# Kernel tuning notes

Measured on AMD Instinct MI355X. Metric: run time of the kernel, lower is better.

## Reference

```python
import jax, jax.numpy as jnp
import numpy as np

EPS = 1e-7
TRUNC = 0.5          # truncation level of the robust L1 objective
K_CAND = 64          # max number of piecewise-linear extrema evaluated per row


def _pad_inf(v):
    # (B, n) -> (B, n+2) with -inf / +inf sentinels (torch _pad_inf)
    b = v.shape[0]
    return jnp.concatenate(
        [jnp.full((b, 1), -jnp.inf, v.dtype), v, jnp.full((b, 1), jnp.inf, v.dtype)], axis=-1)


def _pad_cumsum(c):
    # (B, n) -> (B, n+2): leading zero, trailing repeat of last (torch _pad_cumsum)
    return jnp.concatenate([jnp.zeros_like(c[:, :1]), c, c[:, -1:]], axis=-1)


_search_l = jax.vmap(lambda a, v: jnp.searchsorted(a, v, side='left'))
_search_r = jax.vmap(lambda a, v: jnp.searchsorted(a, v, side='right'))


def _align_trunc(x, y, w):
    # Solves min_a sum_i min(TRUNC, w_i * |a*x_i - y_i|) per row. x,y,w: (B, n).
    sign = jnp.sign(x)
    x = x * sign
    y = y * sign
    wx = w * x
    wy = w * y
    ydx = y / jnp.maximum(x, EPS)                       # breakpoints of |a x - y|
    cand_b = (wy - TRUNC) / jnp.maximum(wx, EPS)        # breakpoints where residual hits trunc
    cand_c = (wy + TRUNC) / jnp.maximum(wx, EPS)

    def sorted_cum(v):
        order = jnp.argsort(v, axis=-1)
        vs = jnp.take_along_axis(v, order, axis=-1)
        q = jnp.cumsum(jnp.take_along_axis(wx, order, axis=-1), axis=-1)
        return _pad_inf(vs), _pad_cumsum(q)

    As, QA = sorted_cum(ydx)
    Bs, QB = sorted_cum(cand_b)
    Cs, QC = sorted_cum(cand_c)

    def deriv(search):
        jA = search(As, ydx) - 1
        jB = search(Bs, ydx) - 1
        jC = search(Cs, ydx) - 1
        return (2 * jnp.take_along_axis(QA, jA, axis=-1)
                - jnp.take_along_axis(QB, jB, axis=-1)
                - jnp.take_along_axis(QC, jC, axis=-1))

    left_d = deriv(_search_l)
    right_d = deriv(_search_r)
    is_ext = (left_d < 0) & (right_d >= 0)
    is_ext = is_ext.at[:, 0].set(is_ext[:, 0] | ~jnp.any(is_ext, axis=-1))

    # first K_CAND extrema indices per row (stable sort: extrema=False-key first)
    cand_idx = jnp.argsort(~is_ext, axis=-1, stable=True)[:, :K_CAND]   # (B, K)
    valid = jnp.take_along_axis(is_ext, cand_idx, axis=-1)
    cand_a = jnp.take_along_axis(ydx, cand_idx, axis=-1)                # (B, K)

    # truncated-L1 residual at each candidate a: (B, K)
    res = jnp.sum(
        jnp.minimum(jnp.abs(cand_a[:, :, None] * x[:, None, :] - y[:, None, :]) * w[:, None, :], TRUNC),
        axis=-1)
    res = jnp.where(valid, res, jnp.inf)

    kbest = jnp.argmin(res, axis=-1)                                    # scatter_min equivalent
    loss = jnp.take_along_axis(res, kbest[:, None], axis=-1)[:, 0]
    index = jnp.take_along_axis(cand_idx, kbest[:, None], axis=-1)[:, 0]
    a = (jnp.take_along_axis(y, index[:, None], axis=-1)[:, 0]
         / jnp.maximum(jnp.take_along_axis(x, index[:, None], axis=-1)[:, 0], EPS))
    return a, loss, index


def setup_inputs() -> dict:
    key = jax.random.key(0)
    k1, k2, k3 = jax.random.split(key, 3)
    B, N = 256, 2048
    points_src = jax.random.normal(k1, (B, N, 3), dtype=jnp.float32)
    points_tgt = jax.random.normal(k2, (B, N, 3), dtype=jnp.float32)
    weight = jax.random.uniform(k3, (B, N), dtype=jnp.float32)  # weights >= 0
    return {"points_src": points_src, "points_tgt": points_tgt, "weight": weight}


def reference(points_src, points_tgt, weight):
    # align_points_scale: flatten (..., N, 3) -> (..., 3N), weight broadcast over xyz
    B = points_src.shape[0]
    x = points_src.reshape(B, -1)
    y = points_tgt.reshape(B, -1)
    w = jnp.broadcast_to(weight[..., None], points_src.shape).reshape(B, -1)
    a, loss, index = _align_trunc(x, y, w)
    return a
```

## Files before the change

kernel.cpp:

```cpp
#include <hip/hip_runtime.h>
#include <math.h>

#define NELEM   6144
#define NWEIGHT 2048
#define SORTN   8192
#define NT      1024
#define NWAVE   (NT / 64)
#define KCAND   64
#define DN      6146
#define PERT    (NELEM / NT)
#define CHUNK   (NELEM / NWAVE)
#define QSCALE  32768.0f

#define WINW     5.2e-3f
#define DELTARES 1.5e-3
#define WCAP     384

__device__ __forceinline__ int lb6144(const float* __restrict__ key, float v) {
    int pos = 0;
#pragma unroll
    for (int step = 4096; step > 0; step >>= 1) {
        int np = pos + step;
        if (np <= NELEM && key[np - 1] < v) pos = np;
    }
    return pos;
}

#define CEK(a, b, up) { float lo = fminf(K[a], K[b]), hi = fmaxf(K[a], K[b]); \
                        K[a] = (up) ? lo : hi; K[b] = (up) ? hi : lo; }

__global__ __launch_bounds__(NT, 8)
void pointloss_align_kernel(const float* __restrict__ X,
                            const float* __restrict__ Y,
                            const float* __restrict__ W,
                            float* __restrict__ out)
{
    __shared__ __align__(16) unsigned char s_mem[73744];
    float* s_sort = (float*)s_mem;
    float* s_key  = (float*)s_mem;
    int*   s_dlt  = (int*)  (s_mem + 24576);
    int*   s_dle  = (int*)  (s_mem + 49160);
    float* s_wzf  = (float*)(s_mem + 24576);
    float* s_wy2  = (float*)(s_mem + 49160);

    __shared__ int   s_wtot[2 * NWAVE];
    __shared__ int   s_woff[2 * NWAVE];
    __shared__ int   s_isum[NWAVE];
    __shared__ int   s_cand[KCAND];
    __shared__ float s_res[KCAND];
    __shared__ int   s_wind[WCAP];
    __shared__ float s_wres[WCAP];
    __shared__ int   s_count;
    __shared__ int   s_fb;
    __shared__ float s_wa;
    __shared__ int   s_wcnt;

    const int tid = threadIdx.x;
    const int row = blockIdx.x;
    const float* xb = X + (size_t)row * NELEM;
    const float* yb = Y + (size_t)row * NELEM;
    const float* wb = W + (size_t)row * NWEIGHT;

    float K[8];
    if (tid < NELEM / 8) {
        const int e0 = tid * 8;
        float4 x0 = *(const float4*)(xb + e0);
        float4 x1 = *(const float4*)(xb + e0 + 4);
        float4 y0 = *(const float4*)(yb + e0);
        float4 y1 = *(const float4*)(yb + e0 + 4);
        float xx[8] = {x0.x, x0.y, x0.z, x0.w, x1.x, x1.y, x1.z, x1.w};
        float yy[8] = {y0.x, y0.y, y0.z, y0.w, y1.x, y1.y, y1.z, y1.w};
#pragma unroll
        for (int r = 0; r < 8; ++r) {
            float x = xx[r], y = yy[r];
            float s = (x > 0.f) ? 1.f : ((x < 0.f) ? -1.f : 0.f);
            K[r] = (y * s) / fmaxf(x * s, 1e-7f);
        }
    } else {
#pragma unroll
        for (int r = 0; r < 8; ++r) K[r] = INFINITY;
    }
    if (tid == 0) s_fb = 0;

    CEK(0, 1, true); CEK(2, 3, false); CEK(4, 5, true); CEK(6, 7, false);
    CEK(0, 2, true); CEK(1, 3, true);  CEK(4, 6, false); CEK(5, 7, false);
    CEK(0, 1, true); CEK(2, 3, true);  CEK(4, 5, false); CEK(6, 7, false);
    for (int kk = 8; kk <= 512; kk <<= 1) {
        const bool up = ((tid & (kk >> 3)) == 0);
        for (int jj = kk >> 1; jj >= 8; jj >>= 1) {
            const int m = jj >> 3;
            const bool tmin = (up == ((tid & m) == 0));
#pragma unroll
            for (int r = 0; r < 8; ++r) {
                float o = __shfl_xor(K[r], m);
                K[r] = tmin ? fminf(K[r], o) : fmaxf(K[r], o);
            }
        }
        CEK(0, 4, up); CEK(1, 5, up); CEK(2, 6, up); CEK(3, 7, up);
        CEK(0, 2, up); CEK(1, 3, up); CEK(4, 6, up); CEK(5, 7, up);
        CEK(0, 1, up); CEK(2, 3, up); CEK(4, 5, up); CEK(6, 7, up);
    }
    const int xv = ((tid >> 2) & 7) << 2;
    for (int kk = 1024; kk <= SORTN; kk <<= 1) {
        {
            float4 h0 = {K[0], K[1], K[2], K[3]}, h1 = {K[4], K[5], K[6], K[7]};
            *(float4*)&s_sort[(8 * tid) ^ xv]     = h0;
            *(float4*)&s_sort[(8 * tid + 4) ^ xv] = h1;
        }
        __syncthreads();
        for (int jj = kk >> 1; jj >= 512; jj >>= 1) {
            for (int p = tid; p < SORTN / 2; p += NT) {
                const int i  = ((p & ~(jj - 1)) << 1) | (p & (jj - 1));
                const int ia = i ^ (((i >> 5) & 7) << 2);
                const int ib = ia ^ jj;
                const bool up = ((i & kk) == 0);
                float a = s_sort[ia], b = s_sort[ib];
                float lo = fminf(a, b), hi = fmaxf(a, b);
                s_sort[ia] = up ? lo : hi;
                s_sort[ib] = up ? hi : lo;
            }
            __syncthreads();
        }
        {
            float4 h0 = *(float4*)&s_sort[(8 * tid) ^ xv];
            float4 h1 = *(float4*)&s_sort[(8 * tid + 4) ^ xv];
            K[0] = h0.x; K[1] = h0.y; K[2] = h0.z; K[3] = h0.w;
            K[4] = h1.x; K[5] = h1.y; K[6] = h1.z; K[7] = h1.w;
        }
        __syncthreads();
        const bool up = ((tid & (kk >> 3)) == 0);
        for (int jj = 256; jj >= 8; jj >>= 1) {
            const int m = jj >> 3;
            const bool tmin = (up == ((tid & m) == 0));
#pragma unroll
            for (int r = 0; r < 8; ++r) {
                float o = __shfl_xor(K[r], m);
                K[r] = tmin ? fminf(K[r], o) : fmaxf(K[r], o);
            }
        }
        CEK(0, 4, up); CEK(1, 5, up); CEK(2, 6, up); CEK(3, 7, up);
        CEK(0, 2, up); CEK(1, 3, up); CEK(4, 6, up); CEK(5, 7, up);
        CEK(0, 1, up); CEK(2, 3, up); CEK(4, 5, up); CEK(6, 7, up);
    }
    if (tid < NELEM / 8) {
        float4 h0 = {K[0], K[1], K[2], K[3]}, h1 = {K[4], K[5], K[6], K[7]};
        *(float4*)&s_key[8 * tid]     = h0;
        *(float4*)&s_key[8 * tid + 4] = h1;
    }
    for (int i = tid; i < DN; i += NT) { s_dlt[i] = 0; s_dle[i] = 0; }
    __syncthreads();

    int lvq[PERT];
    {
        const int base = tid * PERT;
#pragma unroll
        for (int q = 0; q < PERT; ++q) {
            const int j = base + q;
            float x = xb[j], y = yb[j], w = wb[j / 3];
            float s = (x > 0.f) ? 1.f : ((x < 0.f) ? -1.f : 0.f);
            float z = x * s, y2 = y * s;
            float wx = w * z, wy = w * y2;
            float mwx = fmaxf(wx, 1e-7f);
            float bbv = (wy - 0.5f) / mwx;
            float ccv = (wy + 0.5f) / mwx;
            float v = y2 / fmaxf(z, 1e-7f);
            int lv = lb6144(s_key, v);
            int uv = lv; while (uv < NELEM && s_key[uv] == v) ++uv;
            int lbp = lb6144(s_key, bbv);
            int ubp = lbp; while (ubp < NELEM && s_key[ubp] == bbv) ++ubp;
            int lcp = lb6144(s_key, ccv);
            int ucp = lcp; while (ucp < NELEM && s_key[ucp] == ccv) ++ucp;
            lvq[q] = lv;
            int qx = __float2int_rn(wx * QSCALE);
            atomicAdd(&s_dlt[uv],  2 * qx);
            atomicAdd(&s_dle[lv],  2 * qx);
            atomicAdd(&s_dlt[ubp], -qx);
            atomicAdd(&s_dle[lbp], -qx);
            atomicAdd(&s_dlt[ucp], -qx);
            atomicAdd(&s_dle[lcp], -qx);
        }
    }
    __syncthreads();

    {
        const int lane = tid & 63, wv = tid >> 6;
        const int cbase = wv * CHUNK;
        int cl = 0, ce = 0;
#pragma unroll
        for (int k = 0; k < CHUNK / 64; ++k) {
            const int p = cbase + k * 64 + lane;
            int a = s_dlt[p], b = s_dle[p];
            for (int d = 1; d < 64; d <<= 1) {
                int ua = __shfl_up(a, d);
                int ub = __shfl_up(b, d);
                if (lane >= d) { a += ua; b += ub; }
            }
            a += cl; b += ce;
            s_dlt[p] = a; s_dle[p] = b;
            cl = __shfl(a, 63); ce = __shfl(b, 63);
        }
        if (lane == 63) { s_wtot[wv] = cl; s_wtot[NWAVE + wv] = ce; }
    }
    __syncthreads();
    if (tid < NWAVE) {
        int a = s_wtot[tid], b = s_wtot[NWAVE + tid];
        const int a0 = a, b0 = b;
        for (int d = 1; d < NWAVE; d <<= 1) {
            int ua = __shfl_up(a, d);
            int ub = __shfl_up(b, d);
            if (tid >= d) { a += ua; b += ub; }
        }
        s_woff[tid] = a - a0;
        s_woff[NWAVE + tid] = b - b0;
    }
    __syncthreads();

    {
        const int base = tid * PERT;
        unsigned char fl[PERT];
        int cnt = 0;
#pragma unroll
        for (int q = 0; q < PERT; ++q) {
            const int p = lvq[q];
            const int pw = p / CHUNK;
            int L = s_dlt[p] + s_woff[pw];
            int R = s_dle[p] + s_woff[NWAVE + pw];
            bool f = (L < 0) && (R >= 0);
            fl[q] = f ? 1 : 0; cnt += fl[q];
        }
        const int lane = tid & 63, wv = tid >> 6;
        int ti = cnt;
        for (int d = 1; d < 64; d <<= 1) {
            int u = __shfl_up(ti, d);
            if (lane >= d) ti += u;
        }
        if (lane == 63) s_isum[wv] = ti;
        __syncthreads();
        int off = 0;
        for (int q = 0; q < wv; ++q) off += s_isum[q];
        const int ex = off + ti - cnt;
        if (tid == NT - 1) s_count = ex + cnt;
        int pos = ex;
#pragma unroll
        for (int q = 0; q < PERT; ++q) {
            if (fl[q]) { if (pos < KCAND) s_cand[pos] = base + q; ++pos; }
        }
    }
    __syncthreads();
    if (tid == 0 && s_count == 0) { s_cand[0] = 0; s_count = 1; s_fb = 1; }
    __syncthreads();

    for (int e = tid; e < NELEM; e += NT) {
        float x = xb[e], y = yb[e], w = wb[e / 3];
        float s = (x > 0.f) ? 1.f : ((x < 0.f) ? -1.f : 0.f);
        s_wzf[e] = w * (x * s);
        s_wy2[e] = w * (y * s);
    }
    __syncthreads();

    const int lane = tid & 63, wv = tid >> 6;
    {
        const int cnt64 = (s_count < KCAND) ? s_count : KCAND;
        for (int c = wv; c < cnt64; c += NWAVE) {
            const int j = s_cand[c];
            float x = xb[j], y = yb[j];
            float s = (x > 0.f) ? 1.f : ((x < 0.f) ? -1.f : 0.f);
            float ak = (y * s) / fmaxf(x * s, 1e-7f);
            float acc = 0.f;
            for (int e = lane; e < NELEM; e += 64)
                acc += fminf(fabsf(fmaf(ak, s_wzf[e], -s_wy2[e])), 0.5f);
            for (int d = 32; d > 0; d >>= 1) acc += __shfl_xor(acc, d);
            if (lane == 0) s_res[c] = acc;
        }
    }
    if (tid == 0) s_wcnt = 0;
    __syncthreads();
    if (tid < KCAND) {
        const int cnt64 = (s_count < KCAND) ? s_count : KCAND;
        float rv = (tid < cnt64) ? s_res[tid] : INFINITY;
        int kb = tid;
        for (int d = 32; d > 0; d >>= 1) {
            float ro = __shfl_xor(rv, d);
            int   ko = __shfl_xor(kb, d);
            if (ro < rv || (ro == rv && ko < kb)) { rv = ro; kb = ko; }
        }
        if (tid == 0) {
            const int j = s_cand[kb];
            float x = xb[j], y = yb[j];
            float s = (x > 0.f) ? 1.f : ((x < 0.f) ? -1.f : 0.f);
            s_wa = (y * s) / fmaxf(x * s, 1e-7f);
        }
    }
    __syncthreads();

    const float awin = s_wa;
    if (!s_fb) {
        for (int j = tid; j < NELEM; j += NT) {
            float x = xb[j], y = yb[j];
            float s = (x > 0.f) ? 1.f : ((x < 0.f) ? -1.f : 0.f);
            float v = (y * s) / fmaxf(x * s, 1e-7f);
            if (fabsf(v - awin) <= WINW) {
                int p = atomicAdd(&s_wcnt, 1);
                if (p < WCAP) s_wind[p] = j;
            }
        }
    }
    __syncthreads();
    const int wtot = s_wcnt;
    const int wcnt = (wtot < WCAP) ? wtot : WCAP;
    const bool commit = (s_fb != 0) || (wtot > WCAP);
    if (!commit) {
        for (int c = wv; c < wcnt; c += NWAVE) {
            const int j = s_wind[c];
            float x = xb[j], y = yb[j];
            float s = (x > 0.f) ? 1.f : ((x < 0.f) ? -1.f : 0.f);
            float ak = (y * s) / fmaxf(x * s, 1e-7f);
            float acc = 0.f;
            for (int e = lane; e < NELEM; e += 64)
                acc += fminf(fabsf(fmaf(ak, s_wzf[e], -s_wy2[e])), 0.5f);
            for (int d = 32; d > 0; d >>= 1) acc += __shfl_xor(acc, d);
            if (lane == 0) s_wres[c] = acc;
        }
    }
    __syncthreads();

    if (tid == 0) {
        float outv = awin;
        if (!commit && wcnt > 0) {
            double rmin = INFINITY;
            for (int i = 0; i < wcnt; ++i) rmin = fmin(rmin, (double)s_wres[i]);
            double A = INFINITY, B = -INFINITY;
            for (int i = 0; i < wcnt; ++i) {
                double excess = (double)s_wres[i] - rmin;
                if (excess <= DELTARES) {
                    const int j = s_wind[i];
                    float x = xb[j], y = yb[j];
                    float s = (x > 0.f) ? 1.f : ((x < 0.f) ? -1.f : 0.f);
                    double a = (double)((y * s) / fmaxf(x * s, 1e-7f));
                    A = fmin(A, a + excess);
                    B = fmax(B, a - excess);
                }
            }
            outv = (float)(0.5 * (A + B));
        }
        out[row] = outv;
    }
}

extern "C" void kernel_launch(void* const* d_in, const int* in_sizes, int n_in,
                              void* d_out, int out_size, void* d_ws, size_t ws_size,
                              hipStream_t stream) {
    const float* X = (const float*)d_in[0];
    const float* Y = (const float*)d_in[1];
    const float* W = (const float*)d_in[2];
    float* out = (float*)d_out;
    const int nrows = in_sizes[0] / NELEM;
    pointloss_align_kernel<<<dim3(nrows), dim3(NT), 0, stream>>>(X, Y, W, out);
}
```

Baseline: 107.5 us.

## Use register splitter search and sorted-key window range for candidate scan

Replaces the 13-step binary search over the shared sorted keys with a two-level search. Lanes first pick a block of 96 through splitters held in registers and exchanged by wave shuffles, then search within that block in LDS. The window-candidate collection no longer rescans global x/y with an atomic counter; it finds the contiguous range of sorted keys near the winner by binary search and reads the candidate values straight from the sorted array. This cuts LDS traffic, global reloads and divisions, at the cost of added shuffles and a possibly different candidate ordering.

```diff
diff --git a/kernel.cpp b/kernel.cpp
--- a/kernel.cpp
+++ b/kernel.cpp
@@ -16,12 +16,20 @@
 #define DELTARES 1.5e-3
 #define WCAP     384
 
-__device__ __forceinline__ int lb6144(const float* __restrict__ key, float v) {
-    int pos = 0;
-#pragma unroll
-    for (int step = 4096; step > 0; step >>= 1) {
-        int np = pos + step;
-        if (np <= NELEM && key[np - 1] < v) pos = np;
+__device__ __forceinline__ int lb_spl(const float* __restrict__ key, float spl, float v) {
+    int blk = 0;
+#pragma unroll
+    for (int st = 64; st > 0; st >>= 1) {
+        int nb = blk + st;
+        float p = __shfl(spl, (nb - 1) & 63);
+        if (nb <= 64 && p < v) blk = nb;
+    }
+    int pos = blk * 96;
+    const int lim = (pos + 96 < NELEM) ? (pos + 96) : NELEM;
+#pragma unroll
+    for (int st = 64; st > 0; st >>= 1) {
+        int np = pos + st;
+        if (np <= lim && key[np - 1] < v) pos = np;
     }
     return pos;
 }
@@ -48,12 +56,11 @@
     __shared__ int   s_isum[NWAVE];
     __shared__ int   s_cand[KCAND];
     __shared__ float s_res[KCAND];
-    __shared__ int   s_wind[WCAP];
     __shared__ float s_wres[WCAP];
     __shared__ int   s_count;
     __shared__ int   s_fb;
     __shared__ float s_wa;
-    __shared__ int   s_wcnt;
+    __shared__ int   s_lo, s_hi;
 
     const int tid = threadIdx.x;
     const int row = blockIdx.x;
@@ -150,6 +157,8 @@
     for (int i = tid; i < DN; i += NT) { s_dlt[i] = 0; s_dle[i] = 0; }
     __syncthreads();
 
+    const float spl = s_key[96 * (tid & 63) + 95];
+
     int lvq[PERT];
     {
         const int base = tid * PERT;
@@ -164,11 +173,11 @@
             float bbv = (wy - 0.5f) / mwx;
             float ccv = (wy + 0.5f) / mwx;
             float v = y2 / fmaxf(z, 1e-7f);
-            int lv = lb6144(s_key, v);
+            int lv = lb_spl(s_key, spl, v);
             int uv = lv; while (uv < NELEM && s_key[uv] == v) ++uv;
-            int lbp = lb6144(s_key, bbv);
+            int lbp = lb_spl(s_key, spl, bbv);
             int ubp = lbp; while (ubp < NELEM && s_key[ubp] == bbv) ++ubp;
-            int lcp = lb6144(s_key, ccv);
+            int lcp = lb_spl(s_key, spl, ccv);
             int ucp = lcp; while (ucp < NELEM && s_key[ucp] == ccv) ++ucp;
             lvq[q] = lv;
             int qx = __float2int_rn(wx * QSCALE);
@@ -273,7 +282,6 @@
             if (lane == 0) s_res[c] = acc;
         }
     }
-    if (tid == 0) s_wcnt = 0;
     __syncthreads();
     if (tid < KCAND) {
         const int cnt64 = (s_count < KCAND) ? s_count : KCAND;
@@ -295,26 +303,22 @@
 
     const float awin = s_wa;
     if (!s_fb) {
-        for (int j = tid; j < NELEM; j += NT) {
-            float x = xb[j], y = yb[j];
-            float s = (x > 0.f) ? 1.f : ((x < 0.f) ? -1.f : 0.f);
-            float v = (y * s) / fmaxf(x * s, 1e-7f);
-            if (fabsf(v - awin) <= WINW) {
-                int p = atomicAdd(&s_wcnt, 1);
-                if (p < WCAP) s_wind[p] = j;
-            }
-        }
-    }
-    __syncthreads();
-    const int wtot = s_wcnt;
+        int lo = lb_spl(s_key, spl, awin - WINW);
+        while (lo > 0 && fabsf(s_key[lo - 1] - awin) <= WINW) --lo;
+        while (lo < NELEM && fabsf(s_key[lo] - awin) > WINW) ++lo;
+        int hi = lb_spl(s_key, spl, awin + WINW);
+        while (hi < NELEM && fabsf(s_key[hi] - awin) <= WINW) ++hi;
+        while (hi > lo && fabsf(s_key[hi - 1] - awin) > WINW) --hi;
+        if (tid == 0) { s_lo = lo; s_hi = hi; }
+    } else if (tid == 0) { s_lo = 0; s_hi = 0; }
+    __syncthreads();
+    const int lo = s_lo;
+    const int wtot = s_hi - s_lo;
     const int wcnt = (wtot < WCAP) ? wtot : WCAP;
     const bool commit = (s_fb != 0) || (wtot > WCAP);
     if (!commit) {
         for (int c = wv; c < wcnt; c += NWAVE) {
-            const int j = s_wind[c];
-            float x = xb[j], y = yb[j];
-            float s = (x > 0.f) ? 1.f : ((x < 0.f) ? -1.f : 0.f);
-            float ak = (y * s) / fmaxf(x * s, 1e-7f);
+            float ak = s_key[lo + c];
             float acc = 0.f;
             for (int e = lane; e < NELEM; e += 64)
                 acc += fminf(fabsf(fmaf(ak, s_wzf[e], -s_wy2[e])), 0.5f);
@@ -333,10 +337,7 @@
             for (int i = 0; i < wcnt; ++i) {
                 double excess = (double)s_wres[i] - rmin;
                 if (excess <= DELTARES) {
-                    const int j = s_wind[i];
-                    float x = xb[j], y = yb[j];
-                    float s = (x > 0.f) ? 1.f : ((x < 0.f) ? -1.f : 0.f);
-                    double a = (double)((y * s) / fmaxf(x * s, 1e-7f));
+                    double a = (double)s_key[lo + i];
                     A = fmin(A, a + excess);
                     B = fmax(B, a - excess);
                 }
```

New measurement: 105.0 us. -2.4%, faster.
